# Kernel tuning notes

Hardware: AMD Instinct MI355X
Metric: run time of the kernel (lower is better)

The kernel has to match this reference:

```python
import jax, jax.numpy as jnp
import numpy as np

B, S, H = 1, 1024, 2048
E, F, FS = 32, 768, 4096
TOP_K = 4
SCALE = 0.02


def setup_inputs() -> dict:
    key = jax.random.key(0)
    ks = jax.random.split(key, 9)
    return {
        "hidden_states": jax.random.normal(ks[0], (B, S, H), jnp.float32),
        "router_weight": jax.random.normal(ks[1], (E, H), jnp.float32) * SCALE,
        "w_gate": jax.random.normal(ks[2], (E, H, F), jnp.float32) * SCALE,
        "w_up": jax.random.normal(ks[3], (E, H, F), jnp.float32) * SCALE,
        "w_down": jax.random.normal(ks[4], (E, F, H), jnp.float32) * SCALE,
        "sw_gate": jax.random.normal(ks[5], (H, FS), jnp.float32) * SCALE,
        "sw_up": jax.random.normal(ks[6], (H, FS), jnp.float32) * SCALE,
        "sw_down": jax.random.normal(ks[7], (FS, H), jnp.float32) * SCALE,
        "sgate_w": jax.random.normal(ks[8], (H, 1), jnp.float32) * SCALE,
    }


def reference(hidden_states, router_weight, w_gate, w_up, w_down,
              sw_gate, sw_up, sw_down, sgate_w):
    b, s, h = hidden_states.shape
    x = hidden_states.reshape(-1, h)                      # [T,H]
    T = x.shape[0]

    # ---- router: linear -> softmax (fp32) -> topk -> renormalize ----
    logits = x @ router_weight.T                          # [T,E]
    probs = jax.nn.softmax(logits.astype(jnp.float32), axis=-1)
    topv, topi = jax.lax.top_k(probs, TOP_K)              # [T,K]
    topv = topv / jnp.sum(topv, axis=-1, keepdims=True)
    topv = topv.astype(probs.dtype)

    # combine weights: scatter topk weights into dense [T,E] mask
    combine = jnp.zeros((T, E), probs.dtype).at[
        jnp.arange(T)[:, None], topi].add(topv)

    # ---- experts: SwiGLU per expert, weighted combine ----
    g = jnp.einsum('th,ehf->etf', x, w_gate)              # [E,T,F]
    u = jnp.einsum('th,ehf->etf', x, w_up)                # [E,T,F]
    act = jax.nn.silu(g) * u                              # [E,T,F]
    out = jnp.einsum('te,etf,efh->th', combine, act, w_down)  # [T,H]

    # ---- shared expert with sigmoid gate ----
    shared = (jax.nn.silu(x @ sw_gate) * (x @ sw_up)) @ sw_down  # [T,H]
    out = out + jax.nn.sigmoid(x @ sgate_w) * shared

    return out.reshape(b, s, h)
```

## Files before the change

kernel.cpp:

```cpp
#include <hip/hip_runtime.h>
#include <math.h>

#define T_TOK 1024
#define H_DIM 2048
#define N_EXP 32
#define TOPK  4
#define F_DIM 768
#define FS_DIM 4096
#define FS_HALF 2048

typedef __bf16 bf16;
typedef __attribute__((ext_vector_type(4))) __bf16 bf16x4;
typedef __attribute__((ext_vector_type(8))) __bf16 bf16x8;
typedef __attribute__((ext_vector_type(4))) float f32x4;

#define BAR() do {                                        \
    asm volatile("s_waitcnt lgkmcnt(0)" ::: "memory");    \
    __builtin_amdgcn_s_barrier();                         \
    __builtin_amdgcn_sched_barrier(0);                    \
  } while (0)

__device__ __forceinline__ int swz(int row, int colB) {
  return row * 64 + (colB ^ (((row >> 2) & 3) << 4));
}

__global__ __launch_bounds__(256) void router_kernel(
    const float* __restrict__ x, const float* __restrict__ rw,
    const float* __restrict__ sgw,
    float* __restrict__ topw, float* __restrict__ sg,
    int* __restrict__ counts, int* __restrict__ lists)
{
  int t = blockIdx.x; int tid = threadIdx.x;
  int lane = tid & 63, wave = tid >> 6;
  float acc[N_EXP];
  #pragma unroll
  for (int e = 0; e < N_EXP; e++) acc[e] = 0.f;
  float accs = 0.f;
  const float* xr = x + (size_t)t * H_DIM;
  for (int h = tid; h < H_DIM; h += 256) {
    float xv = xr[h];
    accs += xv * sgw[h];
    #pragma unroll
    for (int e = 0; e < N_EXP; e++) acc[e] += xv * rw[e * H_DIM + h];
  }
  __shared__ float red[4][N_EXP];
  __shared__ float reds[4];
  __shared__ float logits[N_EXP];
  #pragma unroll
  for (int e = 0; e < N_EXP; e++) {
    float v = acc[e];
    for (int off = 32; off; off >>= 1) v += __shfl_down(v, off, 64);
    if (lane == 0) red[wave][e] = v;
  }
  {
    float v = accs;
    for (int off = 32; off; off >>= 1) v += __shfl_down(v, off, 64);
    if (lane == 0) reds[wave] = v;
  }
  __syncthreads();
  if (tid < N_EXP) logits[tid] = red[0][tid] + red[1][tid] + red[2][tid] + red[3][tid];
  __syncthreads();
  if (tid == 0) {
    float m = -1e30f;
    #pragma unroll
    for (int e = 0; e < N_EXP; e++) m = fmaxf(m, logits[e]);
    float p[N_EXP];
    #pragma unroll
    for (int e = 0; e < N_EXP; e++) p[e] = expf(logits[e] - m);
    int ids[TOPK]; float vs[TOPK]; float wsum = 0.f;
    #pragma unroll
    for (int k = 0; k < TOPK; k++) {
      int best = 0; float bv = -1.f;
      for (int e = 0; e < N_EXP; e++) {
        if (p[e] > bv) { bv = p[e]; best = e; }
      }
      ids[k] = best; vs[k] = bv; wsum += bv; p[best] = -2.f;
    }
    float inv = 1.f / wsum;
    float sgs = reds[0] + reds[1] + reds[2] + reds[3];
    sg[t] = 1.f / (1.f + expf(-sgs));
    #pragma unroll
    for (int k = 0; k < TOPK; k++) {
      int slot = t * TOPK + k;
      topw[slot] = vs[k] * inv;
      int pos = atomicAdd(&counts[ids[k]], 1);
      lists[ids[k] * T_TOK + pos] = slot;
    }
  }
}

__global__ __launch_bounds__(256) void xcvt_kernel(
    const float* __restrict__ x, bf16* __restrict__ xb)
{
  size_t i = ((size_t)blockIdx.x * 256 + threadIdx.x) * 8;
  f32x4 a = *(const f32x4*)(x + i);
  f32x4 b = *(const f32x4*)(x + i + 4);
  bf16x8 o;
  #pragma unroll
  for (int j = 0; j < 4; j++) { o[j] = (bf16)a[j]; o[4 + j] = (bf16)b[j]; }
  *(bf16x8*)(xb + i) = o;
}

__global__ __launch_bounds__(512) __attribute__((amdgpu_waves_per_eu(4, 4)))
void gateup_fused(
    const bf16* __restrict__ XB,
    const float* __restrict__ wg_, const float* __restrict__ wu_,
    const float* __restrict__ swg, const float* __restrict__ swu,
    bf16* __restrict__ act, bf16* __restrict__ acts,
    const int* __restrict__ lists, const int* __restrict__ counts,
    int n_shared, int sh_nfb, int actsN, int col_off)
{
  int id = blockIdx.x;
  bool gather = id >= n_shared;
  const float *Wg, *Wu; const int* lb = nullptr;
  int count, mt, fb, ldb, Nout; bf16* C;
  if (gather) {
    int g = id - n_shared;
    int j = g >> 3;
    int e = (g & 7) + 8 * (j / 96);
    int rr = j % 96;
    mt = (rr / 6) * 64; fb = (rr % 6) * 128;
    count = counts[e]; lb = lists + e * T_TOK;
    Wg = wg_ + (size_t)e * H_DIM * F_DIM;
    Wu = wu_ + (size_t)e * H_DIM * F_DIM;
    ldb = F_DIM; Nout = F_DIM; C = act;
  } else {
    fb = (id % sh_nfb) * 128; mt = (id / sh_nfb) * 64;
    count = T_TOK; ldb = FS_DIM; Nout = actsN;
    Wg = swg + col_off; Wu = swu + col_off;
    C = acts;
  }
  if (mt >= count) return;

  __shared__ alignas(16) char sA [2][64 * 64];
  __shared__ alignas(16) char sBg[2][128 * 64];
  __shared__ alignas(16) char sBu[2][128 * 64];

  int tid = threadIdx.x;
  int lane = tid & 63, wid = tid >> 6;
  int wr = wid >> 2, wc = wid & 3;
  int l15 = lane & 15, qB = (lane >> 4) << 4;

  const bf16* aptr;
  {
    int r = mt + (tid >> 3);
    int rc = r < count ? r : count - 1;
    int tok = gather ? (lb[rc] >> 2) : rc;
    aptr = XB + (size_t)tok * H_DIM + ((tid & 7) << 2);
  }
  int t8 = tid & 255;
  int bng = t8 & 31;
  int bk4 = (t8 >> 5) << 2;
  const float* bptr = (tid < 256 ? Wg : Wu) + (size_t)bk4 * ldb + fb + bng * 4;
  char* bds = (tid < 256) ? &sBg[0][0] : &sBu[0][0];

  f32x4 accg[2][2], accu[2][2];
  #pragma unroll
  for (int m = 0; m < 2; m++)
    #pragma unroll
    for (int n = 0; n < 2; n++) {
      accg[m][n] = (f32x4){0.f,0.f,0.f,0.f};
      accu[m][n] = (f32x4){0.f,0.f,0.f,0.f};
    }

  uint2 ava, avb; f32x4 bva[4], bvb[4];

  #define GU_ISSUE(av, bv, k0) do {                                   \
    av = *(const uint2*)(aptr + (k0));                                \
    _Pragma("unroll")                                                 \
    for (int r_ = 0; r_ < 4; r_++)                                    \
      bv[r_] = *(const f32x4*)(bptr + (size_t)((k0) + r_) * ldb);     \
    __builtin_amdgcn_sched_barrier(0);                                \
  } while (0)

  #define GU_STAGE(b, av, bv) do {                                    \
    *(uint2*)(sA[b] + swz(tid >> 3, (tid & 7) << 3)) = av;            \
    _Pragma("unroll")                                                 \
    for (int i_ = 0; i_ < 4; i_++) {                                  \
      bf16x4 tb;                                                      \
      tb[0]=(bf16)bv[0][i_]; tb[1]=(bf16)bv[1][i_];                   \
      tb[2]=(bf16)bv[2][i_]; tb[3]=(bf16)bv[3][i_];                   \
      *(bf16x4*)(bds + (b) * (128 * 64) + swz(bng * 4 + i_, bk4 << 1)) = tb; \
    } } while (0)

  #define GU_MFMA(b) do {                                             \
    __builtin_amdgcn_s_setprio(1);                                    \
    bf16x8 af0 = *(const bf16x8*)(sA[b] + swz(wr * 32 + l15, qB));    \
    bf16x8 af1 = *(const bf16x8*)(sA[b] + swz(wr * 32 + 16 + l15, qB)); \
    _Pragma("unroll")                                                 \
    for (int n_ = 0; n_ < 2; n_++) {                                  \
      int rb = wc * 32 + n_ * 16 + l15;                               \
      bf16x8 bg = *(const bf16x8*)(sBg[b] + swz(rb, qB));             \
      bf16x8 bu = *(const bf16x8*)(sBu[b] + swz(rb, qB));             \
      accg[0][n_] = __builtin_amdgcn_mfma_f32_16x16x32_bf16(af0, bg, accg[0][n_], 0,0,0); \
      accg[1][n_] = __builtin_amdgcn_mfma_f32_16x16x32_bf16(af1, bg, accg[1][n_], 0,0,0); \
      accu[0][n_] = __builtin_amdgcn_mfma_f32_16x16x32_bf16(af0, bu, accu[0][n_], 0,0,0); \
      accu[1][n_] = __builtin_amdgcn_mfma_f32_16x16x32_bf16(af1, bu, accu[1][n_], 0,0,0); \
    }                                                                 \
    __builtin_amdgcn_s_setprio(0);                                    \
  } while (0)

  const int NT = H_DIM / 32;
  GU_ISSUE(ava, bva, 0);
  GU_ISSUE(avb, bvb, 32);
  GU_STAGE(0, ava, bva);
  GU_ISSUE(ava, bva, 64);
  BAR();
  for (int t = 0; t < NT; t += 2) {
    GU_MFMA(0);
    GU_STAGE(1, avb, bvb);
    if (t + 3 < NT) GU_ISSUE(avb, bvb, (t + 3) * 32);
    BAR();
    GU_MFMA(1);
    if (t + 2 < NT) {
      GU_STAGE(0, ava, bva);
      if (t + 4 < NT) GU_ISSUE(ava, bva, (t + 4) * 32);
    }
    BAR();
  }
  #undef GU_ISSUE
  #undef GU_STAGE
  #undef GU_MFMA

  #pragma unroll
  for (int m = 0; m < 2; m++) {
    #pragma unroll
    for (int q = 0; q < 4; q++) {
      int gr = mt + wr * 32 + m * 16 + (lane >> 4) * 4 + q;
      if (gr < count) {
        size_t rowo = (gather ? (size_t)lb[gr] : (size_t)gr) * Nout;
        #pragma unroll
        for (int n = 0; n < 2; n++) {
          float g = accg[m][n][q], u = accu[m][n][q];
          C[rowo + fb + wc * 32 + n * 16 + l15] =
              (bf16)(g / (1.f + __expf(-g)) * u);
        }
      }
    }
  }
}

__global__ __launch_bounds__(256, 4) void dn_shared(
    const bf16* __restrict__ acts, const float* __restrict__ swd,
    float* __restrict__ out, const float* __restrict__ sg,
    int lda_sh, int kd_sh, int swd_off, int accum)
{
  int id = blockIdx.x;
  int nb = (id & 15) * 128, mt = (id >> 4) * 64;
  const bf16* A = acts; int lda = lda_sh, Kd = kd_sh;
  const float* W = swd + (size_t)swd_off * H_DIM;

  __shared__ alignas(16) char sA[2][64 * 64];
  __shared__ alignas(16) char sB[2][128 * 64];

  int tid = threadIdx.x;
  int lane = tid & 63, wid = tid >> 6;
  int wr = wid >> 1, wc = wid & 1;
  int l15 = lane & 15, qB = (lane >> 4) << 4;
  int bng = tid & 31;
  int bk4 = (tid >> 5) << 2;

  const bf16* aptr = A + (size_t)(mt + (tid >> 2)) * lda + ((tid & 3) << 3);
  const float* bptr = W + (size_t)bk4 * H_DIM + nb + bng * 4;

  f32x4 acc[2][4];
  #pragma unroll
  for (int m = 0; m < 2; m++)
    #pragma unroll
    for (int n = 0; n < 4; n++)
      acc[m][n] = (f32x4){0.f,0.f,0.f,0.f};

  uint4 ava, avb; f32x4 bva[4], bvb[4];

  #define DN_ISSUE(av, bv, k0) do {                                   \
    av = *(const uint4*)(aptr + (k0));                                \
    _Pragma("unroll")                                                 \
    for (int r_ = 0; r_ < 4; r_++)                                    \
      bv[r_] = *(const f32x4*)(bptr + (size_t)((k0) + r_) * H_DIM);   \
    } while (0)

  #define DN_STAGE(b, av, bv) do {                                    \
    *(uint4*)(sA[b] + swz(tid >> 2, (tid & 3) << 4)) = av;            \
    _Pragma("unroll")                                                 \
    for (int i_ = 0; i_ < 4; i_++) {                                  \
      bf16x4 tb;                                                      \
      tb[0]=(bf16)bv[0][i_]; tb[1]=(bf16)bv[1][i_];                   \
      tb[2]=(bf16)bv[2][i_]; tb[3]=(bf16)bv[3][i_];                   \
      *(bf16x4*)(sB[b] + swz(bng * 4 + i_, bk4 << 1)) = tb;           \
    } } while (0)

  #define DN_MFMA(b) do {                                             \
    __builtin_amdgcn_s_setprio(1);                                    \
    bf16x8 af0 = *(const bf16x8*)(sA[b] + swz(wr * 32 + l15, qB));    \
    bf16x8 af1 = *(const bf16x8*)(sA[b] + swz(wr * 32 + 16 + l15, qB)); \
    _Pragma("unroll")                                                 \
    for (int n_ = 0; n_ < 4; n_++) {                                  \
      bf16x8 bb = *(const bf16x8*)(sB[b] + swz(wc * 64 + n_ * 16 + l15, qB)); \
      acc[0][n_] = __builtin_amdgcn_mfma_f32_16x16x32_bf16(af0, bb, acc[0][n_], 0,0,0); \
      acc[1][n_] = __builtin_amdgcn_mfma_f32_16x16x32_bf16(af1, bb, acc[1][n_], 0,0,0); \
    }                                                                 \
    __builtin_amdgcn_s_setprio(0);                                    \
  } while (0)

  const int NT = Kd / 32;
  DN_ISSUE(ava, bva, 0);
  DN_ISSUE(avb, bvb, 32);
  DN_STAGE(0, ava, bva);
  DN_ISSUE(ava, bva, 64);
  BAR();
  for (int t = 0; t < NT; t += 2) {
    DN_MFMA(0);
    DN_STAGE(1, avb, bvb);
    if (t + 3 < NT) DN_ISSUE(avb, bvb, (t + 3) * 32);
    BAR();
    DN_MFMA(1);
    if (t + 2 < NT) {
      DN_STAGE(0, ava, bva);
      if (t + 4 < NT) DN_ISSUE(ava, bva, (t + 4) * 32);
    }
    BAR();
  }
  #undef DN_ISSUE
  #undef DN_STAGE
  #undef DN_MFMA

  #pragma unroll
  for (int m = 0; m < 2; m++) {
    #pragma unroll
    for (int q = 0; q < 4; q++) {
      int gr = mt + wr * 32 + m * 16 + (lane >> 4) * 4 + q;
      #pragma unroll
      for (int n = 0; n < 4; n++) {
        int col = nb + wc * 64 + n * 16 + l15;
        if (!accum) out[(size_t)gr * H_DIM + col] = sg[gr] * acc[m][n][q];
        else        out[(size_t)gr * H_DIM + col] += sg[gr] * acc[m][n][q];
      }
    }
  }
}

__global__ __launch_bounds__(256, 4) void dn_expert(
    const bf16* __restrict__ act, const float* __restrict__ wd_,
    bf16* __restrict__ dslot,
    const int* __restrict__ lists, const int* __restrict__ counts)
{
  int g = blockIdx.x;
  int j = g >> 3;
  int e = (g & 7) + 8 * (j >> 7);
  int rr = j & 127;
  int nb = (rr & 15) * 128;
  int mt = (rr >> 4) * 64;
  int count = counts[e];
  const int* lb = lists + e * T_TOK;
  if (mt >= count) return;
  const float* W = wd_ + (size_t)e * F_DIM * H_DIM;

  __shared__ alignas(16) char sA[2][64 * 64];
  __shared__ alignas(16) char sB[2][128 * 64];

  int tid = threadIdx.x;
  int lane = tid & 63, wid = tid >> 6;
  int wr = wid >> 1, wc = wid & 1;
  int l15 = lane & 15, qB = (lane >> 4) << 4;
  int bng = tid & 31;
  int bk4 = (tid >> 5) << 2;

  const bf16* aptr;
  {
    int r = mt + (tid >> 2);
    int rc = r < count ? r : count - 1;
    aptr = act + (size_t)lb[rc] * F_DIM + ((tid & 3) << 3);
  }
  const float* bptr = W + (size_t)bk4 * H_DIM + nb + bng * 4;

  f32x4 acc[2][4];
  #pragma unroll
  for (int m = 0; m < 2; m++)
    #pragma unroll
    for (int n = 0; n < 4; n++)
      acc[m][n] = (f32x4){0.f,0.f,0.f,0.f};

  uint4 ava, avb; f32x4 bva[4], bvb[4];

  #define DE_ISSUE(av, bv, k0) do {                                   \
    av = *(const uint4*)(aptr + (k0));                                \
    _Pragma("unroll")                                                 \
    for (int r_ = 0; r_ < 4; r_++)                                    \
      bv[r_] = *(const f32x4*)(bptr + (size_t)((k0) + r_) * H_DIM);   \
    } while (0)

  #define DE_STAGE(b, av, bv) do {                                    \
    *(uint4*)(sA[b] + swz(tid >> 2, (tid & 3) << 4)) = av;            \
    _Pragma("unroll")                                                 \
    for (int i_ = 0; i_ < 4; i_++) {                                  \
      bf16x4 tb;                                                      \
      tb[0]=(bf16)bv[0][i_]; tb[1]=(bf16)bv[1][i_];                   \
      tb[2]=(bf16)bv[2][i_]; tb[3]=(bf16)bv[3][i_];                   \
      *(bf16x4*)(sB[b] + swz(bng * 4 + i_, bk4 << 1)) = tb;           \
    } } while (0)

  #define DE_MFMA(b) do {                                             \
    __builtin_amdgcn_s_setprio(1);                                    \
    bf16x8 af0 = *(const bf16x8*)(sA[b] + swz(wr * 32 + l15, qB));    \
    bf16x8 af1 = *(const bf16x8*)(sA[b] + swz(wr * 32 + 16 + l15, qB)); \
    _Pragma("unroll")                                                 \
    for (int n_ = 0; n_ < 4; n_++) {                                  \
      bf16x8 bb = *(const bf16x8*)(sB[b] + swz(wc * 64 + n_ * 16 + l15, qB)); \
      acc[0][n_] = __builtin_amdgcn_mfma_f32_16x16x32_bf16(af0, bb, acc[0][n_], 0,0,0); \
      acc[1][n_] = __builtin_amdgcn_mfma_f32_16x16x32_bf16(af1, bb, acc[1][n_], 0,0,0); \
    }                                                                 \
    __builtin_amdgcn_s_setprio(0);                                    \
  } while (0)

  const int NT = F_DIM / 32;
  DE_ISSUE(ava, bva, 0);
  DE_ISSUE(avb, bvb, 32);
  DE_STAGE(0, ava, bva);
  DE_ISSUE(ava, bva, 64);
  BAR();
  for (int t = 0; t < NT; t += 2) {
    DE_MFMA(0);
    DE_STAGE(1, avb, bvb);
    if (t + 3 < NT) DE_ISSUE(avb, bvb, (t + 3) * 32);
    BAR();
    DE_MFMA(1);
    if (t + 2 < NT) {
      DE_STAGE(0, ava, bva);
      if (t + 4 < NT) DE_ISSUE(ava, bva, (t + 4) * 32);
    }
    BAR();
  }
  #undef DE_ISSUE
  #undef DE_STAGE
  #undef DE_MFMA

  #pragma unroll
  for (int m = 0; m < 2; m++) {
    #pragma unroll
    for (int q = 0; q < 4; q++) {
      int gr = mt + wr * 32 + m * 16 + (lane >> 4) * 4 + q;
      if (gr < count) {
        #pragma unroll
        for (int n = 0; n < 4; n++) {
          int col = nb + wc * 64 + n * 16 + l15;
          dslot[(size_t)lb[gr] * H_DIM + col] = (bf16)acc[m][n][q];
        }
      }
    }
  }
}

__global__ __launch_bounds__(256) void combine_kernel(
    const bf16* __restrict__ dslot, const float* __restrict__ topw,
    float* __restrict__ out)
{
  int t = blockIdx.x;
  int h = threadIdx.x * 8;
  float w0 = topw[t * 4 + 0], w1 = topw[t * 4 + 1];
  float w2 = topw[t * 4 + 2], w3 = topw[t * 4 + 3];
  bf16x8 a0 = *(const bf16x8*)&dslot[(size_t)(t * 4 + 0) * H_DIM + h];
  bf16x8 a1 = *(const bf16x8*)&dslot[(size_t)(t * 4 + 1) * H_DIM + h];
  bf16x8 a2 = *(const bf16x8*)&dslot[(size_t)(t * 4 + 2) * H_DIM + h];
  bf16x8 a3 = *(const bf16x8*)&dslot[(size_t)(t * 4 + 3) * H_DIM + h];
  f32x4 o0 = *(f32x4*)&out[(size_t)t * H_DIM + h];
  f32x4 o1 = *(f32x4*)&out[(size_t)t * H_DIM + h + 4];
  float o[8] = {o0[0], o0[1], o0[2], o0[3], o1[0], o1[1], o1[2], o1[3]};
  #pragma unroll
  for (int j = 0; j < 8; j++)
    o[j] += w0 * (float)a0[j] + w1 * (float)a1[j] + w2 * (float)a2[j]
          + w3 * (float)a3[j];
  *(f32x4*)&out[(size_t)t * H_DIM + h]     = (f32x4){o[0], o[1], o[2], o[3]};
  *(f32x4*)&out[(size_t)t * H_DIM + h + 4] = (f32x4){o[4], o[5], o[6], o[7]};
}

extern "C" void kernel_launch(void* const* d_in, const int* in_sizes, int n_in,
                              void* d_out, int out_size, void* d_ws, size_t ws_size,
                              hipStream_t stream) {
  const float* x   = (const float*)d_in[0];
  const float* rw  = (const float*)d_in[1];
  const float* wg  = (const float*)d_in[2];
  const float* wu  = (const float*)d_in[3];
  const float* wd  = (const float*)d_in[4];
  const float* swg = (const float*)d_in[5];
  const float* swu = (const float*)d_in[6];
  const float* swd = (const float*)d_in[7];
  const float* sgw = (const float*)d_in[8];
  float* out = (float*)d_out;
  char* ws = (char*)d_ws;

  size_t off = 0;
  int*   counts = (int*)(ws + off); off += 256;
  int*   lists  = (int*)(ws + off); off += (size_t)N_EXP * T_TOK * 4;
  float* topw   = (float*)(ws + off); off += (size_t)T_TOK * TOPK * 4;
  float* sg     = (float*)(ws + off); off += (size_t)T_TOK * 4;
  bf16*  act    = (bf16*)(ws + off); off += (size_t)T_TOK * TOPK * F_DIM * 2;
  size_t dslot_off = off;
  bf16*  xb     = (bf16*)(ws + off); off += (size_t)T_TOK * H_DIM * 2;
  bf16*  acts   = (bf16*)(ws + off); off += (size_t)T_TOK * FS_HALF * 2;
  off = dslot_off + (size_t)T_TOK * TOPK * H_DIM * 2;
  bf16*  dslot  = (bf16*)(ws + dslot_off);

  hipMemsetAsync(counts, 0, 256, stream);

  router_kernel<<<T_TOK, 256, 0, stream>>>(x, rw, sgw, topw, sg, counts, lists);
  xcvt_kernel<<<(T_TOK * H_DIM) / 2048, 256, 0, stream>>>(x, xb);

  const int SH_NFB = FS_HALF / 128;
  const int NSH_GU = SH_NFB * (T_TOK / 64);
  const int EXP_GU = N_EXP * 96;

  gateup_fused<<<NSH_GU + EXP_GU, 512, 0, stream>>>(
      xb, wg, wu, swg, swu, act, acts, lists, counts,
      NSH_GU, SH_NFB, FS_HALF, 0);
  dn_shared<<<256, 256, 0, stream>>>(acts, swd, out, sg, FS_HALF, FS_HALF, 0, 0);
  gateup_fused<<<NSH_GU, 512, 0, stream>>>(
      xb, wg, wu, swg, swu, act, acts, lists, counts,
      NSH_GU, SH_NFB, FS_HALF, FS_HALF);
  dn_shared<<<256, 256, 0, stream>>>(acts, swd, out, sg, FS_HALF, FS_HALF, FS_HALF, 1);

  dn_expert<<<N_EXP * 128, 256, 0, stream>>>(act, wd, dslot, lists, counts);
  combine_kernel<<<T_TOK, 256, 0, stream>>>(dslot, topw, out);
}
```

Baseline: 428.6 us.

## Merge shared-expert halves into single gate/up and down launches

The shared expert was previously computed in two halves, each with its own gate/up launch and down-projection launch, the second accumulating into the output. Now one gate/up launch covers all 4096 shared columns plus the routed experts, writing into two half-buffers, and one down kernel loops over both K halves and writes the output once. The workspace is re-laid out so that xb and the second shared half alias the dslot region, which is written only later. This removes two launches, the read-modify-write of the output, and the small second gate/up grid, at the cost of a longer K loop per down block and a larger single gate/up grid.

```diff
diff --git a/kernel.cpp b/kernel.cpp
--- a/kernel.cpp
+++ b/kernel.cpp
@@ -102,33 +102,35 @@
 }
 
 __global__ __launch_bounds__(512) __attribute__((amdgpu_waves_per_eu(4, 4)))
-void gateup_fused(
+void gateup_xb(
     const bf16* __restrict__ XB,
     const float* __restrict__ wg_, const float* __restrict__ wu_,
     const float* __restrict__ swg, const float* __restrict__ swu,
-    bf16* __restrict__ act, bf16* __restrict__ acts,
+    bf16* __restrict__ act, bf16* __restrict__ acts0, bf16* __restrict__ acts1,
     const int* __restrict__ lists, const int* __restrict__ counts,
-    int n_shared, int sh_nfb, int actsN, int col_off)
+    int n_shared)
 {
   int id = blockIdx.x;
   bool gather = id >= n_shared;
   const float *Wg, *Wu; const int* lb = nullptr;
-  int count, mt, fb, ldb, Nout; bf16* C;
+  int count, mt, fb, cb, ldb, Nout; bf16* C;
   if (gather) {
     int g = id - n_shared;
     int j = g >> 3;
     int e = (g & 7) + 8 * (j / 96);
     int rr = j % 96;
-    mt = (rr / 6) * 64; fb = (rr % 6) * 128;
+    mt = (rr / 6) * 64; fb = (rr % 6) * 128; cb = fb;
     count = counts[e]; lb = lists + e * T_TOK;
     Wg = wg_ + (size_t)e * H_DIM * F_DIM;
     Wu = wu_ + (size_t)e * H_DIM * F_DIM;
     ldb = F_DIM; Nout = F_DIM; C = act;
   } else {
-    fb = (id % sh_nfb) * 128; mt = (id / sh_nfb) * 64;
-    count = T_TOK; ldb = FS_DIM; Nout = actsN;
-    Wg = swg + col_off; Wu = swu + col_off;
-    C = acts;
+    int fbi = id & 31;
+    mt = (id >> 5) * 64;
+    fb = fbi * 128; cb = (fbi & 15) * 128;
+    count = T_TOK; ldb = FS_DIM; Nout = FS_HALF;
+    Wg = swg; Wu = swu;
+    C = (fbi < 16) ? acts0 : acts1;
   }
   if (mt >= count) return;
 
@@ -232,7 +234,7 @@
         #pragma unroll
         for (int n = 0; n < 2; n++) {
           float g = accg[m][n][q], u = accu[m][n][q];
-          C[rowo + fb + wc * 32 + n * 16 + l15] =
+          C[rowo + cb + wc * 32 + n * 16 + l15] =
               (bf16)(g / (1.f + __expf(-g)) * u);
         }
       }
@@ -240,15 +242,13 @@
   }
 }
 
-__global__ __launch_bounds__(256, 4) void dn_shared(
-    const bf16* __restrict__ acts, const float* __restrict__ swd,
-    float* __restrict__ out, const float* __restrict__ sg,
-    int lda_sh, int kd_sh, int swd_off, int accum)
+__global__ __launch_bounds__(256, 4) void dn_shared2(
+    const bf16* __restrict__ acts0, const bf16* __restrict__ acts1,
+    const float* __restrict__ swd, float* __restrict__ out,
+    const float* __restrict__ sg)
 {
   int id = blockIdx.x;
   int nb = (id & 15) * 128, mt = (id >> 4) * 64;
-  const bf16* A = acts; int lda = lda_sh, Kd = kd_sh;
-  const float* W = swd + (size_t)swd_off * H_DIM;
 
   __shared__ alignas(16) char sA[2][64 * 64];
   __shared__ alignas(16) char sB[2][128 * 64];
@@ -260,9 +260,6 @@
   int bng = tid & 31;
   int bk4 = (tid >> 5) << 2;
 
-  const bf16* aptr = A + (size_t)(mt + (tid >> 2)) * lda + ((tid & 3) << 3);
-  const float* bptr = W + (size_t)bk4 * H_DIM + nb + bng * 4;
-
   f32x4 acc[2][4];
   #pragma unroll
   for (int m = 0; m < 2; m++)
@@ -272,14 +269,14 @@
 
   uint4 ava, avb; f32x4 bva[4], bvb[4];
 
-  #define DN_ISSUE(av, bv, k0) do {                                   \
+  #define DS_ISSUE(av, bv, k0) do {                                   \
     av = *(const uint4*)(aptr + (k0));                                \
     _Pragma("unroll")                                                 \
     for (int r_ = 0; r_ < 4; r_++)                                    \
       bv[r_] = *(const f32x4*)(bptr + (size_t)((k0) + r_) * H_DIM);   \
     } while (0)
 
-  #define DN_STAGE(b, av, bv) do {                                    \
+  #define DS_STAGE(b, av, bv) do {                                    \
     *(uint4*)(sA[b] + swz(tid >> 2, (tid & 3) << 4)) = av;            \
     _Pragma("unroll")                                                 \
     for (int i_ = 0; i_ < 4; i_++) {                                  \
@@ -289,7 +286,7 @@
       *(bf16x4*)(sB[b] + swz(bng * 4 + i_, bk4 << 1)) = tb;           \
     } } while (0)
 
-  #define DN_MFMA(b) do {                                             \
+  #define DS_MFMA(b) do {                                             \
     __builtin_amdgcn_s_setprio(1);                                    \
     bf16x8 af0 = *(const bf16x8*)(sA[b] + swz(wr * 32 + l15, qB));    \
     bf16x8 af1 = *(const bf16x8*)(sA[b] + swz(wr * 32 + 16 + l15, qB)); \
@@ -302,27 +299,34 @@
     __builtin_amdgcn_s_setprio(0);                                    \
   } while (0)
 
-  const int NT = Kd / 32;
-  DN_ISSUE(ava, bva, 0);
-  DN_ISSUE(avb, bvb, 32);
-  DN_STAGE(0, ava, bva);
-  DN_ISSUE(ava, bva, 64);
-  BAR();
-  for (int t = 0; t < NT; t += 2) {
-    DN_MFMA(0);
-    DN_STAGE(1, avb, bvb);
-    if (t + 3 < NT) DN_ISSUE(avb, bvb, (t + 3) * 32);
+  const int NT = FS_HALF / 32;
+  #pragma unroll 1
+  for (int p = 0; p < 2; p++) {
+    const bf16* A = p ? acts1 : acts0;
+    const bf16* aptr = A + (size_t)(mt + (tid >> 2)) * FS_HALF + ((tid & 3) << 3);
+    const float* bptr = swd + (size_t)(p * FS_HALF + bk4) * H_DIM + nb + bng * 4;
+
+    DS_ISSUE(ava, bva, 0);
+    DS_ISSUE(avb, bvb, 32);
+    DS_STAGE(0, ava, bva);
+    DS_ISSUE(ava, bva, 64);
     BAR();
-    DN_MFMA(1);
-    if (t + 2 < NT) {
-      DN_STAGE(0, ava, bva);
-      if (t + 4 < NT) DN_ISSUE(ava, bva, (t + 4) * 32);
-    }
-    BAR();
-  }
-  #undef DN_ISSUE
-  #undef DN_STAGE
-  #undef DN_MFMA
+    for (int t = 0; t < NT; t += 2) {
+      DS_MFMA(0);
+      DS_STAGE(1, avb, bvb);
+      if (t + 3 < NT) DS_ISSUE(avb, bvb, (t + 3) * 32);
+      BAR();
+      DS_MFMA(1);
+      if (t + 2 < NT) {
+        DS_STAGE(0, ava, bva);
+        if (t + 4 < NT) DS_ISSUE(ava, bva, (t + 4) * 32);
+      }
+      BAR();
+    }
+  }
+  #undef DS_ISSUE
+  #undef DS_STAGE
+  #undef DS_MFMA
 
   #pragma unroll
   for (int m = 0; m < 2; m++) {
@@ -332,8 +336,7 @@
       #pragma unroll
       for (int n = 0; n < 4; n++) {
         int col = nb + wc * 64 + n * 16 + l15;
-        if (!accum) out[(size_t)gr * H_DIM + col] = sg[gr] * acc[m][n][q];
-        else        out[(size_t)gr * H_DIM + col] += sg[gr] * acc[m][n][q];
+        out[(size_t)gr * H_DIM + col] = sg[gr] * acc[m][n][q];
       }
     }
   }
@@ -494,30 +497,23 @@
   float* topw   = (float*)(ws + off); off += (size_t)T_TOK * TOPK * 4;
   float* sg     = (float*)(ws + off); off += (size_t)T_TOK * 4;
   bf16*  act    = (bf16*)(ws + off); off += (size_t)T_TOK * TOPK * F_DIM * 2;
-  size_t dslot_off = off;
-  bf16*  xb     = (bf16*)(ws + off); off += (size_t)T_TOK * H_DIM * 2;
-  bf16*  acts   = (bf16*)(ws + off); off += (size_t)T_TOK * FS_HALF * 2;
-  off = dslot_off + (size_t)T_TOK * TOPK * H_DIM * 2;
-  bf16*  dslot  = (bf16*)(ws + dslot_off);
+  bf16*  acts0  = (bf16*)(ws + off); off += (size_t)T_TOK * FS_HALF * 2;
+  bf16*  dslot  = (bf16*)(ws + off); off += (size_t)T_TOK * TOPK * H_DIM * 2;
+  bf16*  xb     = dslot;
+  bf16*  acts1  = dslot + (size_t)T_TOK * FS_HALF;
 
   hipMemsetAsync(counts, 0, 256, stream);
 
   router_kernel<<<T_TOK, 256, 0, stream>>>(x, rw, sgw, topw, sg, counts, lists);
   xcvt_kernel<<<(T_TOK * H_DIM) / 2048, 256, 0, stream>>>(x, xb);
 
-  const int SH_NFB = FS_HALF / 128;
-  const int NSH_GU = SH_NFB * (T_TOK / 64);
+  const int NSH_GU = 32 * (T_TOK / 64);
   const int EXP_GU = N_EXP * 96;
-
-  gateup_fused<<<NSH_GU + EXP_GU, 512, 0, stream>>>(
-      xb, wg, wu, swg, swu, act, acts, lists, counts,
-      NSH_GU, SH_NFB, FS_HALF, 0);
-  dn_shared<<<256, 256, 0, stream>>>(acts, swd, out, sg, FS_HALF, FS_HALF, 0, 0);
-  gateup_fused<<<NSH_GU, 512, 0, stream>>>(
-      xb, wg, wu, swg, swu, act, acts, lists, counts,
-      NSH_GU, SH_NFB, FS_HALF, FS_HALF);
-  dn_shared<<<256, 256, 0, stream>>>(acts, swd, out, sg, FS_HALF, FS_HALF, FS_HALF, 1);
-
-  dn_expert<<<N_EXP * 128, 256, 0, stream>>>(act, wd, dslot, lists, counts);
+  const int DN_EXP = N_EXP * 128;
+
+  gateup_xb<<<NSH_GU + EXP_GU, 512, 0, stream>>>(
+      xb, wg, wu, swg, swu, act, acts0, acts1, lists, counts, NSH_GU);
+  dn_shared2<<<256, 256, 0, stream>>>(acts0, acts1, swd, out, sg);
+  dn_expert<<<DN_EXP, 256, 0, stream>>>(act, wd, dslot, lists, counts);
   combine_kernel<<<T_TOK, 256, 0, stream>>>(dslot, topw, out);
 }
```

Result: faster. 410.1 us (-4.3%).
